# Kernel optimization log

Measured on AMD Instinct MI355X. Metric: run time of the kernel, lower is better.

The kernel has to match this reference:

```python
import jax, jax.numpy as jnp
import numpy as np

B, S, D = 4, 1024, 768
H = 12
DK = D // H            # 64
NUM_EMB = 10
MAX_DIST = 100000.0 * 2 ** 0.5
POS_SCALE = 100000.0   # tile positions live in [0, 100000]


def setup_inputs() -> dict:
    key = jax.random.key(0)
    ks = jax.random.split(key, 12)
    query = jax.random.normal(ks[0], (B, S, D), dtype=jnp.float32)
    key_t = jax.random.normal(ks[1], (B, S, D), dtype=jnp.float32)
    value = jax.random.normal(ks[2], (B, S, D), dtype=jnp.float32)
    tile_positions = jax.random.uniform(ks[3], (B, S, 2), dtype=jnp.float32) * POS_SCALE
    # Linear weights, torch layout [out, in]; xavier_uniform init, zero bias
    lim = float(np.sqrt(6.0 / (D + D)))
    Wq = jax.random.uniform(ks[4], (D, D), minval=-lim, maxval=lim, dtype=jnp.float32)
    Wk = jax.random.uniform(ks[5], (D, D), minval=-lim, maxval=lim, dtype=jnp.float32)
    Wv = jax.random.uniform(ks[6], (D, D), minval=-lim, maxval=lim, dtype=jnp.float32)
    bq = jnp.zeros((D,), jnp.float32)
    bk = jnp.zeros((D,), jnp.float32)
    bv = jnp.zeros((D,), jnp.float32)
    emb_k = jax.random.normal(ks[7], (NUM_EMB, DK), dtype=jnp.float32)  # nn.Embedding default N(0,1)
    return {"query": query, "key": key_t, "value": value,
            "tile_positions": tile_positions,
            "Wq": Wq, "bq": bq, "Wk": Wk, "bk": bk, "Wv": Wv, "bv": bv,
            "emb_k": emb_k}


def reference(query, key, value, tile_positions, Wq, bq, Wk, bk, Wv, bv, emb_k):
    b, s, _ = query.shape
    # projections -> [B, H, S, DK]
    q = (query @ Wq.T + bq).reshape(b, s, H, DK).transpose(0, 2, 1, 3)
    k = (key   @ Wk.T + bk).reshape(b, s, H, DK).transpose(0, 2, 1, 3)
    v = (value @ Wv.T + bv).reshape(b, s, H, DK).transpose(0, 2, 1, 3)
    # pairwise distances, normalized, discretized to embedding indices
    pos = jax.lax.stop_gradient(tile_positions)
    diff = pos[:, :, None, :] - pos[:, None, :, :]          # [B,S,S,2]
    dist = jnp.sqrt(jnp.sum(diff * diff, axis=-1)) / MAX_DIST  # [B,S,S]
    idx = jnp.clip(jnp.round(dist * (NUM_EMB - 1)), 0, NUM_EMB - 1).astype(jnp.int32)
    rk = emb_k[idx]                                          # [B,S,S,DK]
    # logits: QK^T plus distance-aware key bias
    attn_logits = jnp.einsum('bhqd,bhkd->bhqk', q, k)
    attn_logits = attn_logits + jnp.einsum('bhqd,bqkd->bhqk', q, rk)
    attn_logits = attn_logits / (DK ** 0.5)
    attention = jax.nn.softmax(attn_logits, axis=-1)
    out = jnp.einsum('bhqk,bhkd->bhqd', attention, v)       # [B,H,S,DK]
    out = out.transpose(0, 2, 1, 3).reshape(b, s, -1)       # [B,S,D]
    return out
```

## Files before the change

### kernel.cpp

```cpp
#include <hip/hip_runtime.h>
#include <hip/hip_bf16.h>

#define Bsz 4
#define Ssz 1024
#define Dsz 768
#define Hn 12
#define DKsz 64
#define NUMEMB 10

#define POSF_OFF 64
#define EMBF_OFF 32832
#define IDX_OFF  35392
#define K_OFF    4229696
#define V_OFF    10521152

#define BM 64
#define BN 128
#define BK 32
#define LPAD 40

#define IPAD 80

typedef __attribute__((ext_vector_type(8))) short short8;
typedef __attribute__((ext_vector_type(8))) float float8;
typedef __attribute__((ext_vector_type(4))) float f32x4;
typedef __attribute__((ext_vector_type(4))) unsigned int u32x4;

__device__ __forceinline__ float bfbits2f(short u) {
    union { unsigned int i; float f; } v;
    v.i = ((unsigned int)(unsigned short)u) << 16;
    return v.f;
}
__device__ __forceinline__ unsigned short f2bf_bits(float f) {
    __hip_bfloat16 h = __float2bfloat16(f);
    return *reinterpret_cast<unsigned short*>(&h);
}

template<int CTRL>
__device__ __forceinline__ float dppf(float x) {
    int xi = __float_as_int(x);
    int r = __builtin_amdgcn_update_dpp(xi, xi, CTRL, 0xF, 0xF, true);
    return __int_as_float(r);
}
__device__ __forceinline__ float red_max16(float v) {
    v = fmaxf(v, dppf<0xB1>(v));
    v = fmaxf(v, dppf<0x4E>(v));
    v = fmaxf(v, dppf<0x124>(v));
    v = fmaxf(v, dppf<0x128>(v));
    return v;
}
__device__ __forceinline__ float red_sum16(float v) {
    v += dppf<0xB1>(v);
    v += dppf<0x4E>(v);
    v += dppf<0x124>(v);
    v += dppf<0x128>(v);
    return v;
}

template<bool BF16>
__device__ __forceinline__ float loadf(const void* base, size_t idx) {
    if constexpr (BF16) return __bfloat162float(((const __hip_bfloat16*)base)[idx]);
    else return ((const float*)base)[idx];
}
template<bool BF16>
__device__ __forceinline__ short8 load8bf(const void* base, size_t idx) {
    if constexpr (BF16) {
        return *(const short8*)((const short*)base + idx);
    } else {
        float8 f = *(const float8*)((const float*)base + idx);
        short8 r;
#pragma unroll
        for (int i = 0; i < 8; i++) r[i] = (short)f2bf_bits(f[i]);
        return r;
    }
}

__global__ __launch_bounds__(64) void detect_kernel(
    const unsigned int* __restrict__ q, const unsigned int* __restrict__ p,
    const unsigned int* __restrict__ w, const unsigned int* __restrict__ e,
    int* __restrict__ flags)
{
    const int which = blockIdx.x;
    const unsigned int* ptr = (which == 0) ? q : ((which == 1) ? p : ((which == 2) ? w : e));
    const int n = (which == 3) ? 320 : ((which == 1) ? 4096 : 1024);
    int cnt = 0;
    for (int i = threadIdx.x; i < n; i += 64) {
        const unsigned int ex = (ptr[i] >> 7) & 0xFF;
        cnt += (ex >= 110 && ex <= 145) ? 1 : 0;
    }
#pragma unroll
    for (int off = 1; off < 64; off <<= 1) cnt += __shfl_xor(cnt, off, 64);
    if (threadIdx.x == 0) flags[which] = (2 * cnt > n) ? 1 : 0;
}

__global__ __launch_bounds__(256) void prep_kernel(
    const void* __restrict__ pos, const void* __restrict__ emb,
    const int* __restrict__ flags, float* __restrict__ posf, float* __restrict__ embf)
{
    const bool pb = flags[1] != 0, eb = flags[3] != 0;
    const int t0 = blockIdx.x * 256 + threadIdx.x;
    for (int i = t0; i < Bsz * Ssz * 2; i += 1024)
        posf[i] = pb ? loadf<true>(pos, i) : loadf<false>(pos, i);
    for (int i = t0; i < NUMEMB * DKsz; i += 1024)
        embf[i] = eb ? loadf<true>(emb, i) : loadf<false>(emb, i);
}

__global__ __launch_bounds__(256) void idx_kernel(
    const float* __restrict__ posf, unsigned char* __restrict__ idxb)
{
    const int kt = blockIdx.x, qt = blockIdx.y, b = blockIdx.z;
    const int t = threadIdx.x;
    const int r = t >> 2, cc = t & 3;
    const int q = qt * 64 + r;
    const float qx = posf[((size_t)b * Ssz + q) * 2];
    const float qy = posf[((size_t)b * Ssz + q) * 2 + 1];
    const float MAXD = 141421.35623730951f;
    const int k0 = kt * 64 + cc * 16;
    unsigned int w[4];
#pragma unroll
    for (int g = 0; g < 4; g++) {
        unsigned int acc = 0;
#pragma unroll
        for (int u = 0; u < 4; u++) {
            const int k = k0 + g * 4 + u;
            const float kx = posf[((size_t)b * Ssz + k) * 2];
            const float ky = posf[((size_t)b * Ssz + k) * 2 + 1];
            const float dx = __fsub_rn(qx, kx);
            const float dy = __fsub_rn(qy, ky);
            const float ss = __fadd_rn(__fmul_rn(dx, dx), __fmul_rn(dy, dy));
            const float dist = __fdiv_rn(sqrtf(ss), MAXD);
            const float d9 = __fmul_rn(dist, 9.0f);
            int idx = (int)rintf(d9);
            idx = idx < 0 ? 0 : (idx > NUMEMB - 1 ? NUMEMB - 1 : idx);
            acc |= ((unsigned int)idx) << (8 * u);
        }
        w[g] = acc;
    }
    u32x4 v; v[0] = w[0]; v[1] = w[1]; v[2] = w[2]; v[3] = w[3];
    *(u32x4*)(idxb + ((size_t)(b * Ssz + q)) * Ssz + k0) = v;
}

template<bool XB, bool WB>
__device__ __forceinline__ void proj_body(
    const void* X, const void* W, const void* bias, void* Y, bool ybf,
    int bx, int by, short* As, short* Bs)
{
    const int tid  = threadIdx.x;
    const int wave = tid >> 6;
    const int lane = tid & 63;
    const int l15  = lane & 15;
    const int quad = lane >> 4;
    const int wm = wave & 1;
    const int wn = wave >> 1;
    const int m0 = bx * BM;
    const int n0 = by * BN;

    f32x4 acc[2][4];
#pragma unroll
    for (int i = 0; i < 2; i++)
#pragma unroll
        for (int j = 0; j < 4; j++) acc[i][j] = (f32x4)0.0f;

    const int r0 = tid >> 2;
    const int cc = tid & 3;

    short8 pa  = load8bf<XB>(X, (size_t)(m0 + r0)      * Dsz + cc * 8);
    short8 pb0 = load8bf<WB>(W, (size_t)(n0 + r0)      * Dsz + cc * 8);
    short8 pb1 = load8bf<WB>(W, (size_t)(n0 + 64 + r0) * Dsz + cc * 8);

    for (int kk = 0; kk < Dsz; kk += BK) {
        __syncthreads();
        *(short8*)&As[(r0)      * LPAD + cc * 8] = pa;
        *(short8*)&Bs[(r0)      * LPAD + cc * 8] = pb0;
        *(short8*)&Bs[(64 + r0) * LPAD + cc * 8] = pb1;
        __syncthreads();

        if (kk + BK < Dsz) {
            pa  = load8bf<XB>(X, (size_t)(m0 + r0)      * Dsz + kk + BK + cc * 8);
            pb0 = load8bf<WB>(W, (size_t)(n0 + r0)      * Dsz + kk + BK + cc * 8);
            pb1 = load8bf<WB>(W, (size_t)(n0 + 64 + r0) * Dsz + kk + BK + cc * 8);
        }

        short8 af[2], bf[4];
#pragma unroll
        for (int i = 0; i < 2; i++)
            af[i] = *(const short8*)&As[(wm * 32 + i * 16 + l15) * LPAD + quad * 8];
#pragma unroll
        for (int j = 0; j < 4; j++)
            bf[j] = *(const short8*)&Bs[(wn * 64 + j * 16 + l15) * LPAD + quad * 8];
#pragma unroll
        for (int i = 0; i < 2; i++)
#pragma unroll
            for (int j = 0; j < 4; j++)
                acc[i][j] = __builtin_amdgcn_mfma_f32_16x16x32_bf16(af[i], bf[j], acc[i][j], 0, 0, 0);
    }

#pragma unroll
    for (int j = 0; j < 4; j++) {
        const int n = n0 + wn * 64 + j * 16 + l15;
        const float bv_ = loadf<WB>(bias, n);
#pragma unroll
        for (int i = 0; i < 2; i++) {
#pragma unroll
            for (int r = 0; r < 4; r++) {
                const int m = m0 + wm * 32 + i * 16 + quad * 4 + r;
                const float val = acc[i][j][r] + bv_;
                if (ybf) ((__hip_bfloat16*)Y)[(size_t)m * Dsz + n] = __float2bfloat16(val);
                else     ((float*)Y)[(size_t)m * Dsz + n] = val;
            }
        }
    }
}

__global__ __launch_bounds__(256) void proj_kernel(
    const void* X0, const void* X1, const void* X2,
    const void* Wq, const void* bq, const void* Wk, const void* bk,
    const void* Wv, const void* bv,
    void* Qw, void* Kw, void* Vw, const int* __restrict__ flags)
{
    __shared__ __align__(16) short As[BM * LPAD];
    __shared__ __align__(16) short Bs[BN * LPAD];
    const int z = blockIdx.z;
    const void* X = (z == 0) ? X0 : ((z == 1) ? X1 : X2);
    const void* W = (z == 0) ? Wq : ((z == 1) ? Wk : Wv);
    const void* B = (z == 0) ? bq : ((z == 1) ? bk : bv);
    void* Y = (z == 0) ? Qw : ((z == 1) ? Kw : Vw);
    const bool xb = flags[0] != 0, wb = flags[2] != 0;
    const bool ybf = xb || (z != 0);
    if (xb) { if (wb) proj_body<true , true >(X, W, B, Y, ybf, blockIdx.x, blockIdx.y, As, Bs);
              else    proj_body<true , false>(X, W, B, Y, ybf, blockIdx.x, blockIdx.y, As, Bs); }
    else    { if (wb) proj_body<false, true >(X, W, B, Y, ybf, blockIdx.x, blockIdx.y, As, Bs);
              else    proj_body<false, false>(X, W, B, Y, ybf, blockIdx.x, blockIdx.y, As, Bs); }
}

template<bool QB>
__device__ __forceinline__ void attn_body(
    const void* Qw, const short* __restrict__ Ks, const short* __restrict__ Vs,
    const unsigned char* __restrict__ idxb, const float* __restrict__ embf, void* out,
    unsigned short* Klds, unsigned short* Vtlds, unsigned short* Plds,
    float* qe, unsigned char* Ilds)
{
    const int qt = blockIdx.x, h = blockIdx.y, b = blockIdx.z;
    const int tid  = threadIdx.x;
    const int wave = tid >> 6;
    const int lane = tid & 63;
    const int l15  = lane & 15;
    const int quad = lane >> 4;

    for (int p = tid; p < 64 * NUMEMB; p += 256) {
        const int row = p / NUMEMB, e = p - row * NUMEMB;
        const size_t qoff = ((size_t)b * Ssz + qt * 64 + row) * Dsz + h * DKsz;
        float s = 0.f;
#pragma unroll
        for (int c = 0; c < 8; c++) {
            short8 qv = load8bf<QB>(Qw, qoff + c * 8);
            const float* er = embf + e * DKsz + c * 8;
#pragma unroll
            for (int i = 0; i < 8; i++) s += bfbits2f(qv[i]) * er[i];
        }
        qe[p] = s;
    }

    short8 qfrag[2];
    {
        const size_t qbase = ((size_t)b * Ssz + qt * 64 + wave * 16 + l15) * Dsz + h * DKsz;
        qfrag[0] = load8bf<QB>(Qw, qbase + quad * 8);
        qfrag[1] = load8bf<QB>(Qw, qbase + 32 + quad * 8);
    }

    float m_run[4], l_run[4];
    f32x4 oacc[4];
#pragma unroll
    for (int r = 0; r < 4; r++) { m_run[r] = -1e30f; l_run[r] = 0.f; }
#pragma unroll
    for (int j = 0; j < 4; j++) oacc[j] = (f32x4)0.0f;

    const int srow = tid >> 3, schk = tid & 7;
    const int vp   = tid >> 3;
    const int irow = tid >> 2, ichk = tid & 3;

    short8 pk0, pk1, pv0, pv1;
    u32x4 pidx;
    {
        pk0 = *(const short8*)(Ks + ((size_t)b * Ssz + srow)       * Dsz + h * DKsz + schk * 8);
        pk1 = *(const short8*)(Ks + ((size_t)b * Ssz + 32 + srow)  * Dsz + h * DKsz + schk * 8);
        pv0 = *(const short8*)(Vs + ((size_t)b * Ssz + 2 * vp)     * Dsz + h * DKsz + schk * 8);
        pv1 = *(const short8*)(Vs + ((size_t)b * Ssz + 2 * vp + 1) * Dsz + h * DKsz + schk * 8);
        pidx = *(const u32x4*)(idxb + ((size_t)(b * Ssz + irow)) * Ssz + qt * 64 + ichk * 16);
    }

    for (int it = 0; it < 16; it++) {
        __syncthreads();
        *(short8*)&Klds[(srow)      * 72 + schk * 8] = pk0;
        *(short8*)&Klds[(32 + srow) * 72 + schk * 8] = pk1;
        {
            const int ssw = (2 * vp) ^ (schk << 3);
#pragma unroll
            for (int i = 0; i < 8; i++) {
                const unsigned int dw = (unsigned int)(unsigned short)pv0[i]
                                      | ((unsigned int)(unsigned short)pv1[i] << 16);
                *(unsigned int*)&Vtlds[(schk * 8 + i) * 72 + ssw] = dw;
            }
        }
        *(u32x4*)&Ilds[irow * IPAD + ichk * 16] = pidx;
        __syncthreads();

        if (it + 1 < 16) {
            const size_t kb = ((size_t)b * Ssz + (it + 1) * 64) * Dsz + h * DKsz;
            pk0 = *(const short8*)(Ks + kb + (size_t)srow * Dsz + schk * 8);
            pk1 = *(const short8*)(Ks + kb + (size_t)(32 + srow) * Dsz + schk * 8);
            pv0 = *(const short8*)(Vs + kb + (size_t)(2 * vp) * Dsz + schk * 8);
            pv1 = *(const short8*)(Vs + kb + (size_t)(2 * vp + 1) * Dsz + schk * 8);
            pidx = *(const u32x4*)(idxb + ((size_t)(b * Ssz + (it + 1) * 64 + irow)) * Ssz + qt * 64 + ichk * 16);
        }

        f32x4 sf[4];
#pragma unroll
        for (int j = 0; j < 4; j++) sf[j] = (f32x4)0.0f;
#pragma unroll
        for (int st = 0; st < 2; st++) {
#pragma unroll
            for (int j = 0; j < 4; j++) {
                short8 kb2 = *(const short8*)&Klds[(j * 16 + l15) * 72 + st * 32 + quad * 8];
                sf[j] = __builtin_amdgcn_mfma_f32_16x16x32_bf16(qfrag[st], kb2, sf[j], 0, 0, 0);
            }
        }

        float sv[4][4];
#pragma unroll
        for (int j = 0; j < 4; j++) {
            const unsigned int iw = *(const unsigned int*)&Ilds[(j * 16 + l15) * IPAD + wave * 16 + quad * 4];
#pragma unroll
            for (int r = 0; r < 4; r++) {
                const int m = wave * 16 + quad * 4 + r;
                const int idx = (iw >> (8 * r)) & 0xFF;
                sv[r][j] = (sf[j][r] + qe[m * NUMEMB + idx]) * 0.125f;
            }
        }

        float alpha[4];
#pragma unroll
        for (int r = 0; r < 4; r++) {
            float vmax = fmaxf(fmaxf(sv[r][0], sv[r][1]), fmaxf(sv[r][2], sv[r][3]));
            vmax = red_max16(vmax);
            const float mnew = fmaxf(m_run[r], vmax);
            alpha[r] = __expf(m_run[r] - mnew);
            m_run[r] = mnew;
            float psum = 0.f;
#pragma unroll
            for (int j = 0; j < 4; j++) {
                const float p = __expf(sv[r][j] - mnew);
                sv[r][j] = p;
                psum += p;
            }
            psum = red_sum16(psum);
            l_run[r] = l_run[r] * alpha[r] + psum;
        }
#pragma unroll
        for (int j = 0; j < 4; j++) {
            f32x4 o = oacc[j];
#pragma unroll
            for (int r = 0; r < 4; r++) o[r] *= alpha[r];
            oacc[j] = o;
        }

#pragma unroll
        for (int r = 0; r < 4; r++) {
            const int m = wave * 16 + quad * 4 + r;
#pragma unroll
            for (int j = 0; j < 4; j++) {
                const int csw = (j * 16 + l15) ^ (quad << 4);
                Plds[m * 72 + csw] = f2bf_bits(sv[r][j]);
            }
        }

#pragma unroll
        for (int st = 0; st < 2; st++) {
            const int prow = wave * 16 + l15;
            const int pcsw = (st * 32 + quad * 8) ^ ((l15 >> 2) << 4);
            short8 pf = *(const short8*)&Plds[prow * 72 + pcsw];
#pragma unroll
            for (int j = 0; j < 4; j++) {
                const int d = j * 16 + l15;
                const int vsw = (st * 32 + quad * 8) ^ (((d >> 3) & 7) << 3);
                short8 vb = *(const short8*)&Vtlds[d * 72 + vsw];
                oacc[j] = __builtin_amdgcn_mfma_f32_16x16x32_bf16(pf, vb, oacc[j], 0, 0, 0);
            }
        }
    }

    __syncthreads();

#pragma unroll
    for (int r = 0; r < 4; r++) {
        const float inv = 1.0f / l_run[r];
        const int m = qt * 64 + wave * 16 + quad * 4 + r;
#pragma unroll
        for (int j = 0; j < 4; j++) {
            const int n = h * DKsz + j * 16 + l15;
            const float val = oacc[j][r] * inv;
            const size_t oidx = ((size_t)b * Ssz + m) * Dsz + n;
            if constexpr (QB) ((__hip_bfloat16*)out)[oidx] = __float2bfloat16(val);
            else              ((float*)out)[oidx] = val;
        }
    }
}

__global__ __launch_bounds__(256) void attn_kernel(
    const void* Qw, const short* __restrict__ Ks, const short* __restrict__ Vs,
    const unsigned char* __restrict__ idxb, const float* __restrict__ embf, void* out,
    const int* __restrict__ flags)
{
    __shared__ __align__(16) unsigned short Klds[64 * 72];
    __shared__ __align__(16) unsigned short Vtlds[64 * 72];
    __shared__ __align__(16) unsigned short Plds[64 * 72];
    __shared__ __align__(16) float qe[64 * NUMEMB];
    __shared__ __align__(16) unsigned char Ilds[64 * IPAD];

    if (flags[0] != 0)
        attn_body<true >(Qw, Ks, Vs, idxb, embf, out, Klds, Vtlds, Plds, qe, Ilds);
    else
        attn_body<false>(Qw, Ks, Vs, idxb, embf, out, Klds, Vtlds, Plds, qe, Ilds);
}

extern "C" void kernel_launch(void* const* d_in, const int* in_sizes, int n_in,
                              void* d_out, int out_size, void* d_ws, size_t ws_size,
                              hipStream_t stream) {
    const void* query = d_in[0];
    const void* key   = d_in[1];
    const void* value = d_in[2];
    const void* tpos  = d_in[3];
    const void* Wq    = d_in[4];
    const void* bq    = d_in[5];
    const void* Wk    = d_in[6];
    const void* bk    = d_in[7];
    const void* Wv    = d_in[8];
    const void* bv    = d_in[9];
    const void* emb   = d_in[10];

    int*           flags = (int*)d_ws;
    float*         posf  = (float*)((char*)d_ws + POSF_OFF);
    float*         embf  = (float*)((char*)d_ws + EMBF_OFF);
    unsigned char* idxb  = (unsigned char*)d_ws + IDX_OFF;
    void*          Kw    = (char*)d_ws + K_OFF;
    void*          Vw    = (char*)d_ws + V_OFF;
    void*          Qw    = d_out;

    detect_kernel<<<4, 64, 0, stream>>>(
        (const unsigned int*)query, (const unsigned int*)tpos,
        (const unsigned int*)Wq, (const unsigned int*)emb, flags);

    prep_kernel<<<4, 256, 0, stream>>>(tpos, emb, flags, posf, embf);

    idx_kernel<<<dim3(16, 16, Bsz), 256, 0, stream>>>(posf, idxb);

    proj_kernel<<<dim3(64, 6, 3), 256, 0, stream>>>(
        query, key, value, Wq, bq, Wk, bk, Wv, bv, Qw, Kw, Vw, flags);

    attn_kernel<<<dim3(16, Hn, Bsz), 256, 0, stream>>>(
        Qw, (const short*)Kw, (const short*)Vw, idxb, embf, d_out, flags);
}
```

Measured before the change: 229.7 us.

## Pre-convert inputs and weights to bf16, widen projection K-tile, drop prep kernel

Adds a conversion kernel that writes the fp32 activations and weights to bf16 workspace buffers, chosen by workspace size. The projection GEMM then reads half-width operands and uses a 64-wide K step with two MFMA sub-steps per LDS stage, halving the number of barriers. The prep kernel is removed: idx_kernel reads positions directly and the attention kernel reads the embedding table directly. This trades an extra full read and write pass over the inputs, plus an extra launch, for cheaper GEMM loads.

```diff
diff --git a/kernel.cpp b/kernel.cpp
--- a/kernel.cpp
+++ b/kernel.cpp
@@ -8,16 +8,16 @@
 #define DKsz 64
 #define NUMEMB 10
 
-#define POSF_OFF 64
-#define EMBF_OFF 32832
-#define IDX_OFF  35392
-#define K_OFF    4229696
-#define V_OFF    10521152
-
-#define BM 64
-#define BN 128
-#define BK 32
-#define LPAD 40
+#define IDX_OFF 64
+#define K_OFF   4194368
+#define V_OFF   10485824
+#define WBF_OFF 16777280
+#define XBF_OFF 20316224
+#define WS_TIER_B 20316224ULL
+#define WS_TIER_A 39190592ULL
+
+#define NXz 3145728
+#define NWz 589824
 
 #define IPAD 80
 
@@ -74,6 +74,18 @@
         return r;
     }
 }
+template<bool BF16>
+__device__ __forceinline__ float8 load8f(const void* base, size_t idx) {
+    if constexpr (BF16) {
+        short8 s = *(const short8*)((const short*)base + idx);
+        float8 f;
+#pragma unroll
+        for (int i = 0; i < 8; i++) f[i] = bfbits2f(s[i]);
+        return f;
+    } else {
+        return *(const float8*)((const float*)base + idx);
+    }
+}
 
 __global__ __launch_bounds__(64) void detect_kernel(
     const unsigned int* __restrict__ q, const unsigned int* __restrict__ p,
@@ -93,27 +105,50 @@
     if (threadIdx.x == 0) flags[which] = (2 * cnt > n) ? 1 : 0;
 }
 
-__global__ __launch_bounds__(256) void prep_kernel(
-    const void* __restrict__ pos, const void* __restrict__ emb,
-    const int* __restrict__ flags, float* __restrict__ posf, float* __restrict__ embf)
-{
-    const bool pb = flags[1] != 0, eb = flags[3] != 0;
-    const int t0 = blockIdx.x * 256 + threadIdx.x;
-    for (int i = t0; i < Bsz * Ssz * 2; i += 1024)
-        posf[i] = pb ? loadf<true>(pos, i) : loadf<false>(pos, i);
-    for (int i = t0; i < NUMEMB * DKsz; i += 1024)
-        embf[i] = eb ? loadf<true>(emb, i) : loadf<false>(emb, i);
-}
-
-__global__ __launch_bounds__(256) void idx_kernel(
-    const float* __restrict__ posf, unsigned char* __restrict__ idxb)
+__global__ __launch_bounds__(256) void conv_kernel(
+    const void* __restrict__ X0, const void* __restrict__ X1, const void* __restrict__ X2,
+    const void* __restrict__ W0, const void* __restrict__ W1, const void* __restrict__ W2,
+    const int* __restrict__ flags, short* __restrict__ Xbf, short* __restrict__ Wbf,
+    int doX)
+{
+    const long t = (long)blockIdx.x * 256 + threadIdx.x;
+    const bool xb = flags[0] != 0, wb = flags[2] != 0;
+    if (doX) {
+        const long i8 = t * 8;
+        if (i8 < (long)3 * NXz) {
+            const int z = (int)(i8 / NXz);
+            const long off = i8 - (long)z * NXz;
+            const void* X = (z == 0) ? X0 : ((z == 1) ? X1 : X2);
+            short8 v = xb ? load8bf<true>(X, off) : load8bf<false>(X, off);
+            *(short8*)(Xbf + i8) = v;
+        } else {
+            const long j = i8 - (long)3 * NXz;
+            const int z = (int)(j / NWz);
+            const long off = j - (long)z * NWz;
+            const void* W = (z == 0) ? W0 : ((z == 1) ? W1 : W2);
+            short8 v = wb ? load8bf<true>(W, off) : load8bf<false>(W, off);
+            *(short8*)(Wbf + j) = v;
+        }
+    } else {
+        const long j = t * 8;
+        const int z = (int)(j / NWz);
+        const long off = j - (long)z * NWz;
+        const void* W = (z == 0) ? W0 : ((z == 1) ? W1 : W2);
+        short8 v = wb ? load8bf<true>(W, off) : load8bf<false>(W, off);
+        *(short8*)(Wbf + j) = v;
+    }
+}
+
+template<bool PB>
+__device__ __forceinline__ void idx_body(
+    const void* pos, unsigned char* __restrict__ idxb)
 {
     const int kt = blockIdx.x, qt = blockIdx.y, b = blockIdx.z;
     const int t = threadIdx.x;
     const int r = t >> 2, cc = t & 3;
     const int q = qt * 64 + r;
-    const float qx = posf[((size_t)b * Ssz + q) * 2];
-    const float qy = posf[((size_t)b * Ssz + q) * 2 + 1];
+    const float qx = loadf<PB>(pos, ((size_t)b * Ssz + q) * 2);
+    const float qy = loadf<PB>(pos, ((size_t)b * Ssz + q) * 2 + 1);
     const float MAXD = 141421.35623730951f;
     const int k0 = kt * 64 + cc * 16;
     unsigned int w[4];
@@ -123,8 +158,8 @@
 #pragma unroll
         for (int u = 0; u < 4; u++) {
             const int k = k0 + g * 4 + u;
-            const float kx = posf[((size_t)b * Ssz + k) * 2];
-            const float ky = posf[((size_t)b * Ssz + k) * 2 + 1];
+            const float kx = loadf<PB>(pos, ((size_t)b * Ssz + k) * 2);
+            const float ky = loadf<PB>(pos, ((size_t)b * Ssz + k) * 2 + 1);
             const float dx = __fsub_rn(qx, kx);
             const float dy = __fsub_rn(qy, ky);
             const float ss = __fadd_rn(__fmul_rn(dx, dx), __fmul_rn(dy, dy));
@@ -140,9 +175,16 @@
     *(u32x4*)(idxb + ((size_t)(b * Ssz + q)) * Ssz + k0) = v;
 }
 
+__global__ __launch_bounds__(256) void idx_kernel(
+    const void* pos, const int* __restrict__ flags, unsigned char* __restrict__ idxb)
+{
+    if (flags[1] != 0) idx_body<true >(pos, idxb);
+    else               idx_body<false>(pos, idxb);
+}
+
 template<bool XB, bool WB>
 __device__ __forceinline__ void proj_body(
-    const void* X, const void* W, const void* bias, void* Y, bool ybf,
+    const void* X, const void* W, const void* bias, bool biasbf, void* Y, bool ybf,
     int bx, int by, short* As, short* Bs)
 {
     const int tid  = threadIdx.x;
@@ -152,8 +194,8 @@
     const int quad = lane >> 4;
     const int wm = wave & 1;
     const int wn = wave >> 1;
-    const int m0 = bx * BM;
-    const int n0 = by * BN;
+    const int m0 = bx * 64;
+    const int n0 = by * 128;
 
     f32x4 acc[2][4];
 #pragma unroll
@@ -161,44 +203,57 @@
 #pragma unroll
         for (int j = 0; j < 4; j++) acc[i][j] = (f32x4)0.0f;
 
-    const int r0 = tid >> 2;
-    const int cc = tid & 3;
-
-    short8 pa  = load8bf<XB>(X, (size_t)(m0 + r0)      * Dsz + cc * 8);
+    const int r0 = tid >> 3;
+    const int cc = tid & 7;
+
+    short8 pa0 = load8bf<XB>(X, (size_t)(m0 + r0)      * Dsz + cc * 8);
+    short8 pa1 = load8bf<XB>(X, (size_t)(m0 + 32 + r0) * Dsz + cc * 8);
     short8 pb0 = load8bf<WB>(W, (size_t)(n0 + r0)      * Dsz + cc * 8);
-    short8 pb1 = load8bf<WB>(W, (size_t)(n0 + 64 + r0) * Dsz + cc * 8);
-
-    for (int kk = 0; kk < Dsz; kk += BK) {
+    short8 pb1 = load8bf<WB>(W, (size_t)(n0 + 32 + r0) * Dsz + cc * 8);
+    short8 pb2 = load8bf<WB>(W, (size_t)(n0 + 64 + r0) * Dsz + cc * 8);
+    short8 pb3 = load8bf<WB>(W, (size_t)(n0 + 96 + r0) * Dsz + cc * 8);
+
+    for (int kk = 0; kk < Dsz; kk += 64) {
         __syncthreads();
-        *(short8*)&As[(r0)      * LPAD + cc * 8] = pa;
-        *(short8*)&Bs[(r0)      * LPAD + cc * 8] = pb0;
-        *(short8*)&Bs[(64 + r0) * LPAD + cc * 8] = pb1;
+        *(short8*)&As[(r0)      * 72 + cc * 8] = pa0;
+        *(short8*)&As[(32 + r0) * 72 + cc * 8] = pa1;
+        *(short8*)&Bs[(r0)      * 72 + cc * 8] = pb0;
+        *(short8*)&Bs[(32 + r0) * 72 + cc * 8] = pb1;
+        *(short8*)&Bs[(64 + r0) * 72 + cc * 8] = pb2;
+        *(short8*)&Bs[(96 + r0) * 72 + cc * 8] = pb3;
         __syncthreads();
 
-        if (kk + BK < Dsz) {
-            pa  = load8bf<XB>(X, (size_t)(m0 + r0)      * Dsz + kk + BK + cc * 8);
-            pb0 = load8bf<WB>(W, (size_t)(n0 + r0)      * Dsz + kk + BK + cc * 8);
-            pb1 = load8bf<WB>(W, (size_t)(n0 + 64 + r0) * Dsz + kk + BK + cc * 8);
-        }
-
-        short8 af[2], bf[4];
-#pragma unroll
-        for (int i = 0; i < 2; i++)
-            af[i] = *(const short8*)&As[(wm * 32 + i * 16 + l15) * LPAD + quad * 8];
-#pragma unroll
-        for (int j = 0; j < 4; j++)
-            bf[j] = *(const short8*)&Bs[(wn * 64 + j * 16 + l15) * LPAD + quad * 8];
-#pragma unroll
-        for (int i = 0; i < 2; i++)
+        if (kk + 64 < Dsz) {
+            const int k2 = kk + 64 + cc * 8;
+            pa0 = load8bf<XB>(X, (size_t)(m0 + r0)      * Dsz + k2);
+            pa1 = load8bf<XB>(X, (size_t)(m0 + 32 + r0) * Dsz + k2);
+            pb0 = load8bf<WB>(W, (size_t)(n0 + r0)      * Dsz + k2);
+            pb1 = load8bf<WB>(W, (size_t)(n0 + 32 + r0) * Dsz + k2);
+            pb2 = load8bf<WB>(W, (size_t)(n0 + 64 + r0) * Dsz + k2);
+            pb3 = load8bf<WB>(W, (size_t)(n0 + 96 + r0) * Dsz + k2);
+        }
+
+#pragma unroll
+        for (int st = 0; st < 2; st++) {
+            short8 af[2], bf[4];
+#pragma unroll
+            for (int i = 0; i < 2; i++)
+                af[i] = *(const short8*)&As[(wm * 32 + i * 16 + l15) * 72 + st * 32 + quad * 8];
 #pragma unroll
             for (int j = 0; j < 4; j++)
-                acc[i][j] = __builtin_amdgcn_mfma_f32_16x16x32_bf16(af[i], bf[j], acc[i][j], 0, 0, 0);
+                bf[j] = *(const short8*)&Bs[(wn * 64 + j * 16 + l15) * 72 + st * 32 + quad * 8];
+#pragma unroll
+            for (int i = 0; i < 2; i++)
+#pragma unroll
+                for (int j = 0; j < 4; j++)
+                    acc[i][j] = __builtin_amdgcn_mfma_f32_16x16x32_bf16(af[i], bf[j], acc[i][j], 0, 0, 0);
+        }
     }
 
 #pragma unroll
     for (int j = 0; j < 4; j++) {
         const int n = n0 + wn * 64 + j * 16 + l15;
-        const float bv_ = loadf<WB>(bias, n);
+        const float bv_ = biasbf ? loadf<true>(bias, n) : loadf<false>(bias, n);
 #pragma unroll
         for (int i = 0; i < 2; i++) {
 #pragma unroll
@@ -216,27 +271,30 @@
     const void* X0, const void* X1, const void* X2,
     const void* Wq, const void* bq, const void* Wk, const void* bk,
     const void* Wv, const void* bv,
-    void* Qw, void* Kw, void* Vw, const int* __restrict__ flags)
-{
-    __shared__ __align__(16) short As[BM * LPAD];
-    __shared__ __align__(16) short Bs[BN * LPAD];
+    void* Qw, void* Kw, void* Vw, const int* __restrict__ flags,
+    int fx, int fw)
+{
+    __shared__ __align__(16) short As[64 * 72];
+    __shared__ __align__(16) short Bs[128 * 72];
     const int z = blockIdx.z;
     const void* X = (z == 0) ? X0 : ((z == 1) ? X1 : X2);
     const void* W = (z == 0) ? Wq : ((z == 1) ? Wk : Wv);
     const void* B = (z == 0) ? bq : ((z == 1) ? bk : bv);
     void* Y = (z == 0) ? Qw : ((z == 1) ? Kw : Vw);
-    const bool xb = flags[0] != 0, wb = flags[2] != 0;
-    const bool ybf = xb || (z != 0);
-    if (xb) { if (wb) proj_body<true , true >(X, W, B, Y, ybf, blockIdx.x, blockIdx.y, As, Bs);
-              else    proj_body<true , false>(X, W, B, Y, ybf, blockIdx.x, blockIdx.y, As, Bs); }
-    else    { if (wb) proj_body<false, true >(X, W, B, Y, ybf, blockIdx.x, blockIdx.y, As, Bs);
-              else    proj_body<false, false>(X, W, B, Y, ybf, blockIdx.x, blockIdx.y, As, Bs); }
-}
-
-template<bool QB>
+    const bool xb = fx || flags[0] != 0;
+    const bool wb = fw || flags[2] != 0;
+    const bool biasbf = flags[2] != 0;
+    const bool ybf = (flags[0] != 0) || (z != 0);
+    if (xb) { if (wb) proj_body<true , true >(X, W, B, biasbf, Y, ybf, blockIdx.x, blockIdx.y, As, Bs);
+              else    proj_body<true , false>(X, W, B, biasbf, Y, ybf, blockIdx.x, blockIdx.y, As, Bs); }
+    else    { if (wb) proj_body<false, true >(X, W, B, biasbf, Y, ybf, blockIdx.x, blockIdx.y, As, Bs);
+              else    proj_body<false, false>(X, W, B, biasbf, Y, ybf, blockIdx.x, blockIdx.y, As, Bs); }
+}
+
+template<bool QB, bool EB>
 __device__ __forceinline__ void attn_body(
     const void* Qw, const short* __restrict__ Ks, const short* __restrict__ Vs,
-    const unsigned char* __restrict__ idxb, const float* __restrict__ embf, void* out,
+    const unsigned char* __restrict__ idxb, const void* __restrict__ emb, void* out,
     unsigned short* Klds, unsigned short* Vtlds, unsigned short* Plds,
     float* qe, unsigned char* Ilds)
 {
@@ -254,9 +312,9 @@
 #pragma unroll
         for (int c = 0; c < 8; c++) {
             short8 qv = load8bf<QB>(Qw, qoff + c * 8);
-            const float* er = embf + e * DKsz + c * 8;
-#pragma unroll
-            for (int i = 0; i < 8; i++) s += bfbits2f(qv[i]) * er[i];
+            float8 ef = load8f<EB>(emb, (size_t)e * DKsz + c * 8);
+#pragma unroll
+            for (int i = 0; i < 8; i++) s += bfbits2f(qv[i]) * ef[i];
         }
         qe[p] = s;
     }
@@ -408,7 +466,7 @@
 
 __global__ __launch_bounds__(256) void attn_kernel(
     const void* Qw, const short* __restrict__ Ks, const short* __restrict__ Vs,
-    const unsigned char* __restrict__ idxb, const float* __restrict__ embf, void* out,
+    const unsigned char* __restrict__ idxb, const void* __restrict__ emb, void* out,
     const int* __restrict__ flags)
 {
     __shared__ __align__(16) unsigned short Klds[64 * 72];
@@ -417,10 +475,11 @@
     __shared__ __align__(16) float qe[64 * NUMEMB];
     __shared__ __align__(16) unsigned char Ilds[64 * IPAD];
 
-    if (flags[0] != 0)
-        attn_body<true >(Qw, Ks, Vs, idxb, embf, out, Klds, Vtlds, Plds, qe, Ilds);
-    else
-        attn_body<false>(Qw, Ks, Vs, idxb, embf, out, Klds, Vtlds, Plds, qe, Ilds);
+    const bool qb = flags[0] != 0, eb = flags[3] != 0;
+    if (qb) { if (eb) attn_body<true , true >(Qw, Ks, Vs, idxb, emb, out, Klds, Vtlds, Plds, qe, Ilds);
+              else    attn_body<true , false>(Qw, Ks, Vs, idxb, emb, out, Klds, Vtlds, Plds, qe, Ilds); }
+    else    { if (eb) attn_body<false, true >(Qw, Ks, Vs, idxb, emb, out, Klds, Vtlds, Plds, qe, Ilds);
+              else    attn_body<false, false>(Qw, Ks, Vs, idxb, emb, out, Klds, Vtlds, Plds, qe, Ilds); }
 }
 
 extern "C" void kernel_launch(void* const* d_in, const int* in_sizes, int n_in,
@@ -439,24 +498,42 @@
     const void* emb   = d_in[10];
 
     int*           flags = (int*)d_ws;
-    float*         posf  = (float*)((char*)d_ws + POSF_OFF);
-    float*         embf  = (float*)((char*)d_ws + EMBF_OFF);
     unsigned char* idxb  = (unsigned char*)d_ws + IDX_OFF;
     void*          Kw    = (char*)d_ws + K_OFF;
     void*          Vw    = (char*)d_ws + V_OFF;
+    short*         Wbf   = (short*)((char*)d_ws + WBF_OFF);
+    short*         Xbf   = (short*)((char*)d_ws + XBF_OFF);
     void*          Qw    = d_out;
+
+    const bool tierA = ws_size >= WS_TIER_A;
+    const bool tierB = !tierA && ws_size >= WS_TIER_B;
 
     detect_kernel<<<4, 64, 0, stream>>>(
         (const unsigned int*)query, (const unsigned int*)tpos,
         (const unsigned int*)Wq, (const unsigned int*)emb, flags);
 
-    prep_kernel<<<4, 256, 0, stream>>>(tpos, emb, flags, posf, embf);
-
-    idx_kernel<<<dim3(16, 16, Bsz), 256, 0, stream>>>(posf, idxb);
-
-    proj_kernel<<<dim3(64, 6, 3), 256, 0, stream>>>(
-        query, key, value, Wq, bq, Wk, bk, Wv, bv, Qw, Kw, Vw, flags);
+    if (tierA)
+        conv_kernel<<<5472, 256, 0, stream>>>(query, key, value, Wq, Wk, Wv, flags, Xbf, Wbf, 1);
+    else if (tierB)
+        conv_kernel<<<864, 256, 0, stream>>>(query, key, value, Wq, Wk, Wv, flags, Xbf, Wbf, 0);
+
+    idx_kernel<<<dim3(16, 16, Bsz), 256, 0, stream>>>(tpos, flags, idxb);
+
+    if (tierA)
+        proj_kernel<<<dim3(64, 6, 3), 256, 0, stream>>>(
+            Xbf, Xbf + NXz, Xbf + 2 * NXz,
+            Wbf, bq, Wbf + NWz, bk, Wbf + 2 * NWz, bv,
+            Qw, Kw, Vw, flags, 1, 1);
+    else if (tierB)
+        proj_kernel<<<dim3(64, 6, 3), 256, 0, stream>>>(
+            query, key, value,
+            Wbf, bq, Wbf + NWz, bk, Wbf + 2 * NWz, bv,
+            Qw, Kw, Vw, flags, 0, 1);
+    else
+        proj_kernel<<<dim3(64, 6, 3), 256, 0, stream>>>(
+            query, key, value, Wq, bq, Wk, bk, Wv, bv,
+            Qw, Kw, Vw, flags, 0, 0);
 
     attn_kernel<<<dim3(16, Hn, Bsz), 256, 0, stream>>>(
-        Qw, (const short*)Kw, (const short*)Vw, idxb, embf, d_out, flags);
-}
+        Qw, (const short*)Kw, (const short*)Vw, idxb, emb, d_out, flags);
+}
```

After: 221.0 us. 3.8% less time.
